# Kernel optimization log

Measured on AMD Instinct MI355X. Metric: run time of the kernel, lower is better.

Reference implementation:

```python
import jax, jax.numpy as jnp
import numpy as np


def setup_inputs() -> dict:
    key = jax.random.key(0)
    # coeffs_tensor: stacked/padded wavelet coefficients [B, F, T]
    coeffs = jax.random.normal(key, (16, 256, 8192), dtype=jnp.float32)
    return {"coeffs": coeffs}


def reference(coeffs) -> jnp.ndarray:
    B, F, T = coeffs.shape
    # torch.angle on a real tensor -> 0 for x>=0, pi for x<0; jnp.angle matches.
    phase = jnp.angle(coeffs)
    inst_freq = jnp.diff(phase, axis=-1)
    inst_freq = jnp.pad(inst_freq, ((0, 0), (0, 0), (0, 1)))  # F.pad(..., (0,1))
    freq_adjusted = jnp.clip(inst_freq, -1.0, 1.0)  # [B,F,T]
    # k = (f + freq_adjusted).long(); .long() truncates toward zero, as does astype(int32)
    f_idx = jnp.arange(F, dtype=coeffs.dtype)[None, :, None]
    k = jnp.clip((f_idx + freq_adjusted).astype(jnp.int32), 0, F - 1)  # [B,F,T]
    # Fused scatter-add over all (b, f, t): sst[b, k[b,f,t], t] += coeffs[b, f, t]
    b_idx = jnp.arange(B)[:, None, None]
    t_idx = jnp.arange(T)[None, None, :]
    sst = jnp.zeros_like(coeffs).at[b_idx, k, t_idx].add(coeffs)
    return sst
```

## Files before the change

### kernel.cpp

```cpp
#include <hip/hip_runtime.h>

typedef float f32x4 __attribute__((ext_vector_type(4)));

#define BB 16
#define FF 256
#define TT 8192
#define F_CHUNK 8
#define ROWS (F_CHUNK + 2)
#define THREADS 256
#define TBLK (THREADS * 4)
#define LROW 1024

__device__ __forceinline__ void dma16(const float* g, float* l) {
    __builtin_amdgcn_global_load_lds(
        (const __attribute__((address_space(1))) unsigned int*)g,
        (__attribute__((address_space(3))) unsigned int*)l,
        16, 0, 0);
}

__device__ __forceinline__ int sgn_bit(float x) {
    return (int)(__float_as_uint(x) >> 31);
}

__global__ __launch_bounds__(THREADS) void sst_kernel(const float* __restrict__ in,
                                                      float* __restrict__ out) {
    __shared__ float sm[ROWS][LROW];

    const int tid    = threadIdx.x;
    const int wid    = tid >> 6;
    const int blockT = blockIdx.x * TBLK;
    const int fs     = blockIdx.y * F_CHUNK;
    const int b      = blockIdx.z;

    const float* srcB = in  + (size_t)b * FF * TT + blockT;
    float*       dstB = out + (size_t)b * FF * TT + blockT;

    const bool hasNext = (blockT + TBLK) < TT;
    const bool lastThr = (tid == THREADS - 1);

    #pragma unroll
    for (int i = 0; i < ROWS; ++i) {
        int f = fs - 1 + i;
        f = f < 0 ? 0 : (f > FF - 1 ? FF - 1 : f);
        dma16(srcB + (size_t)f * TT + tid * 4, &sm[i][wid * 256]);
    }

    float eg[ROWS];
    #pragma unroll
    for (int i = 0; i < ROWS; ++i) eg[i] = 0.0f;
    if (lastThr && hasNext) {
        #pragma unroll
        for (int i = 0; i < ROWS; ++i) {
            int f = fs - 1 + i;
            f = f < 0 ? 0 : (f > FF - 1 ? FF - 1 : f);
            eg[i] = srcB[(size_t)f * TT + TBLK];
        }
    }

    asm volatile("s_waitcnt vmcnt(0)" ::: "memory");
    __syncthreads();

    const int  tid4 = tid * 4;
    const bool tail = (blockT + tid4 + 4 >= TT);
    const int  eidx = tid4 + 4 > LROW - 1 ? LROW - 1 : tid4 + 4;

    f32x4    v[ROWS];
    unsigned pk[ROWS];
    #pragma unroll
    for (int i = 0; i < ROWS; ++i) {
        const int f = fs - 1 + i;
        const bool oob = (f < 0) | (f > FF - 1);
        v[i] = *reinterpret_cast<const f32x4*>(&sm[i][tid4]);
        const float el = sm[i][eidx];
        const float e  = lastThr ? eg[i] : el;
        const int s0 = sgn_bit(v[i][0]), s1 = sgn_bit(v[i][1]),
                  s2 = sgn_bit(v[i][2]), s3 = sgn_bit(v[i][3]), s4 = sgn_bit(e);
        const int a0 = s1 - s0 + 1;
        const int a1 = s2 - s1 + 1;
        const int a2 = s3 - s2 + 1;
        const int a3 = tail ? 1 : (s4 - s3 + 1);
        pk[i] = oob ? 0x55u : (unsigned)(a0 | (a1 << 2) | (a2 << 4) | (a3 << 6));
    }

    #pragma unroll
    for (int i = 1; i <= F_CHUNK; ++i) {
        const int g = fs + (i - 1);
        const bool isFirst = (g == 0);
        const bool isLast  = (g == FF - 1);

        const unsigned pp = pk[i - 1], pc = pk[i], pn = pk[i + 1];
        const f32x4    vp = v[i - 1],  vc = v[i],  vn = v[i + 1];

        f32x4 r;
        {
            const unsigned cp = pp & 3u, cc = pc & 3u, cn = pn & 3u;
            const bool bc = (cc == 1u) || (isFirst && cc == 0u) || (isLast && cc == 2u);
            r[0] = ((cp == 2u) ? vp[0] : 0.f) + (bc ? vc[0] : 0.f) + ((cn == 0u) ? vn[0] : 0.f);
        }
        {
            const unsigned cp = (pp >> 2) & 3u, cc = (pc >> 2) & 3u, cn = (pn >> 2) & 3u;
            const bool bc = (cc == 1u) || (isFirst && cc == 0u) || (isLast && cc == 2u);
            r[1] = ((cp == 2u) ? vp[1] : 0.f) + (bc ? vc[1] : 0.f) + ((cn == 0u) ? vn[1] : 0.f);
        }
        {
            const unsigned cp = (pp >> 4) & 3u, cc = (pc >> 4) & 3u, cn = (pn >> 4) & 3u;
            const bool bc = (cc == 1u) || (isFirst && cc == 0u) || (isLast && cc == 2u);
            r[2] = ((cp == 2u) ? vp[2] : 0.f) + (bc ? vc[2] : 0.f) + ((cn == 0u) ? vn[2] : 0.f);
        }
        {
            const unsigned cp = (pp >> 6) & 3u, cc = (pc >> 6) & 3u, cn = (pn >> 6) & 3u;
            const bool bc = (cc == 1u) || (isFirst && cc == 0u) || (isLast && cc == 2u);
            r[3] = ((cp == 2u) ? vp[3] : 0.f) + (bc ? vc[3] : 0.f) + ((cn == 0u) ? vn[3] : 0.f);
        }

        __builtin_nontemporal_store(r, reinterpret_cast<f32x4*>(dstB + (size_t)g * TT + tid4));
    }
}

extern "C" void kernel_launch(void* const* d_in, const int* in_sizes, int n_in,
                              void* d_out, int out_size, void* d_ws, size_t ws_size,
                              hipStream_t stream) {
    const float* in  = (const float*)d_in[0];
    float*       out = (float*)d_out;
    dim3 grid(TT / TBLK, FF / F_CHUNK, BB);
    sst_kernel<<<grid, THREADS, 0, stream>>>(in, out);
}
```

Measured before the change: 225.5 us.

## Pipeline row loads with staged vmcnt waits and defer block-edge column fixup

The single wait for all ten row DMAs is replaced by staged waits (vmcnt 6/5/5), so early rows are processed and stored while later rows are still arriving. The last thread's extra global loads of the next column before the barrier are removed. The final column of each block is first written with a placeholder value and then recomputed by a fixup pass after all loads drain. The risk is that counting outstanding vmcnt across DMA and store operations is fragile, and the fixup adds a second store to the edge column.

```diff
diff --git a/kernel.cpp b/kernel.cpp
--- a/kernel.cpp
+++ b/kernel.cpp
@@ -9,6 +9,7 @@
 #define ROWS (F_CHUNK + 2)
 #define THREADS 256
 #define TBLK (THREADS * 4)
+#define NXBLK (TT / TBLK)
 #define LROW 1024
 
 __device__ __forceinline__ void dma16(const float* g, float* l) {
@@ -28,92 +29,99 @@
 
     const int tid    = threadIdx.x;
     const int wid    = tid >> 6;
+    const int tid4   = tid * 4;
     const int blockT = blockIdx.x * TBLK;
     const int fs     = blockIdx.y * F_CHUNK;
     const int b      = blockIdx.z;
 
-    const float* srcB = in  + (size_t)b * FF * TT + blockT;
-    float*       dstB = out + (size_t)b * FF * TT + blockT;
-
-    const bool hasNext = (blockT + TBLK) < TT;
-    const bool lastThr = (tid == THREADS - 1);
+    const float* srcRow = in  + (size_t)b * FF * TT;
+    float*       dstRow = out + (size_t)b * FF * TT;
 
     #pragma unroll
     for (int i = 0; i < ROWS; ++i) {
         int f = fs - 1 + i;
         f = f < 0 ? 0 : (f > FF - 1 ? FF - 1 : f);
-        dma16(srcB + (size_t)f * TT + tid * 4, &sm[i][wid * 256]);
+        dma16(srcRow + (size_t)f * TT + blockT + tid4, &sm[i][wid * 256]);
+        __builtin_amdgcn_sched_barrier(0);
     }
 
-    float eg[ROWS];
-    #pragma unroll
-    for (int i = 0; i < ROWS; ++i) eg[i] = 0.0f;
-    if (lastThr && hasNext) {
-        #pragma unroll
-        for (int i = 0; i < ROWS; ++i) {
-            int f = fs - 1 + i;
-            f = f < 0 ? 0 : (f > FF - 1 ? FF - 1 : f);
-            eg[i] = srcB[(size_t)f * TT + TBLK];
-        }
-    }
-
-    asm volatile("s_waitcnt vmcnt(0)" ::: "memory");
-    __syncthreads();
-
-    const int  tid4 = tid * 4;
-    const bool tail = (blockT + tid4 + 4 >= TT);
-    const int  eidx = tid4 + 4 > LROW - 1 ? LROW - 1 : tid4 + 4;
+    const int  eidx    = (tid4 + 4 > LROW - 1) ? (LROW - 1) : (tid4 + 4);
+    const bool tailThr = (blockIdx.x == NXBLK - 1) && (tid == THREADS - 1);
 
     f32x4    v[ROWS];
     unsigned pk[ROWS];
-    #pragma unroll
-    for (int i = 0; i < ROWS; ++i) {
-        const int f = fs - 1 + i;
+
+    auto finish_row = [&](int i) {
+        v[i] = *reinterpret_cast<const f32x4*>(&sm[i][tid4]);
+        const float e = sm[i][eidx];
+        const int f   = fs - 1 + i;
         const bool oob = (f < 0) | (f > FF - 1);
-        v[i] = *reinterpret_cast<const f32x4*>(&sm[i][tid4]);
-        const float el = sm[i][eidx];
-        const float e  = lastThr ? eg[i] : el;
         const int s0 = sgn_bit(v[i][0]), s1 = sgn_bit(v[i][1]),
                   s2 = sgn_bit(v[i][2]), s3 = sgn_bit(v[i][3]), s4 = sgn_bit(e);
-        const int a0 = s1 - s0 + 1;
-        const int a1 = s2 - s1 + 1;
-        const int a2 = s3 - s2 + 1;
-        const int a3 = tail ? 1 : (s4 - s3 + 1);
+        const int a0 = s1 - s0 + 1, a1 = s2 - s1 + 1, a2 = s3 - s2 + 1;
+        const int a3 = tailThr ? 1 : (s4 - s3 + 1);
         pk[i] = oob ? 0x55u : (unsigned)(a0 | (a1 << 2) | (a2 << 4) | (a3 << 6));
-    }
+    };
 
-    #pragma unroll
-    for (int i = 1; i <= F_CHUNK; ++i) {
+    auto emit_row = [&](int i) {
         const int g = fs + (i - 1);
-        const bool isFirst = (g == 0);
-        const bool isLast  = (g == FF - 1);
-
+        const bool isFirst = (g == 0), isLast = (g == FF - 1);
         const unsigned pp = pk[i - 1], pc = pk[i], pn = pk[i + 1];
         const f32x4    vp = v[i - 1],  vc = v[i],  vn = v[i + 1];
+        f32x4 r;
+        #pragma unroll
+        for (int q = 0; q < 4; ++q) {
+            const unsigned cp = (pp >> (2 * q)) & 3u;
+            const unsigned cc = (pc >> (2 * q)) & 3u;
+            const unsigned cn = (pn >> (2 * q)) & 3u;
+            const bool bc = (cc == 1u) || (isFirst && cc == 0u) || (isLast && cc == 2u);
+            r[q] = ((cp == 2u) ? vp[q] : 0.f) + (bc ? vc[q] : 0.f) + ((cn == 0u) ? vn[q] : 0.f);
+        }
+        __builtin_nontemporal_store(
+            r, reinterpret_cast<f32x4*>(dstRow + (size_t)g * TT + blockT + tid4));
+    };
 
-        f32x4 r;
-        {
-            const unsigned cp = pp & 3u, cc = pc & 3u, cn = pn & 3u;
-            const bool bc = (cc == 1u) || (isFirst && cc == 0u) || (isLast && cc == 2u);
-            r[0] = ((cp == 2u) ? vp[0] : 0.f) + (bc ? vc[0] : 0.f) + ((cn == 0u) ? vn[0] : 0.f);
+    asm volatile("s_waitcnt vmcnt(6)" ::: "memory");
+    __builtin_amdgcn_s_barrier();
+    __builtin_amdgcn_sched_barrier(0);
+    finish_row(0); finish_row(1); finish_row(2); finish_row(3);
+    emit_row(1); emit_row(2);
+
+    asm volatile("s_waitcnt vmcnt(5)" ::: "memory");
+    __builtin_amdgcn_s_barrier();
+    __builtin_amdgcn_sched_barrier(0);
+    finish_row(4); finish_row(5); finish_row(6);
+    emit_row(3); emit_row(4); emit_row(5);
+
+    asm volatile("s_waitcnt vmcnt(5)" ::: "memory");
+    __builtin_amdgcn_s_barrier();
+    __builtin_amdgcn_sched_barrier(0);
+    finish_row(7); finish_row(8); finish_row(9);
+    emit_row(6); emit_row(7); emit_row(8);
+
+    if (blockIdx.x != NXBLK - 1) {
+        asm volatile("s_waitcnt vmcnt(0)" ::: "memory");
+        __builtin_amdgcn_s_barrier();
+        __builtin_amdgcn_sched_barrier(0);
+        if (tid < F_CHUNK) {
+            const int g = fs + tid;
+            const size_t cg = (size_t)(blockT + TBLK - 1);
+            const float vpv = sm[tid][LROW - 1];
+            const float vcv = sm[tid + 1][LROW - 1];
+            const float vnv = sm[tid + 2][LROW - 1];
+            const float* nc = srcRow + cg + 1;
+            const int am = (g - 1 >= 0)
+                         ? (sgn_bit(nc[(size_t)(g - 1) * TT]) - sgn_bit(vpv)) : 9;
+            const int ac =  sgn_bit(nc[(size_t)g * TT]) - sgn_bit(vcv);
+            const int an = (g + 1 <= FF - 1)
+                         ? (sgn_bit(nc[(size_t)(g + 1) * TT]) - sgn_bit(vnv)) : 9;
+            const bool bcb = (ac == 0) || (g == 0 && ac < 0) || (g == FF - 1 && ac > 0);
+            float r = 0.f;
+            if (am == 1)  r += vpv;
+            if (bcb)      r += vcv;
+            if (an == -1) r += vnv;
+            dstRow[(size_t)g * TT + cg] = r;
         }
-        {
-            const unsigned cp = (pp >> 2) & 3u, cc = (pc >> 2) & 3u, cn = (pn >> 2) & 3u;
-            const bool bc = (cc == 1u) || (isFirst && cc == 0u) || (isLast && cc == 2u);
-            r[1] = ((cp == 2u) ? vp[1] : 0.f) + (bc ? vc[1] : 0.f) + ((cn == 0u) ? vn[1] : 0.f);
-        }
-        {
-            const unsigned cp = (pp >> 4) & 3u, cc = (pc >> 4) & 3u, cn = (pn >> 4) & 3u;
-            const bool bc = (cc == 1u) || (isFirst && cc == 0u) || (isLast && cc == 2u);
-            r[2] = ((cp == 2u) ? vp[2] : 0.f) + (bc ? vc[2] : 0.f) + ((cn == 0u) ? vn[2] : 0.f);
-        }
-        {
-            const unsigned cp = (pp >> 6) & 3u, cc = (pc >> 6) & 3u, cn = (pn >> 6) & 3u;
-            const bool bc = (cc == 1u) || (isFirst && cc == 0u) || (isLast && cc == 2u);
-            r[3] = ((cp == 2u) ? vp[3] : 0.f) + (bc ? vc[3] : 0.f) + ((cn == 0u) ? vn[3] : 0.f);
-        }
-
-        __builtin_nontemporal_store(r, reinterpret_cast<f32x4*>(dstB + (size_t)g * TT + tid4));
     }
 }
 
@@ -122,6 +130,6 @@
                               hipStream_t stream) {
     const float* in  = (const float*)d_in[0];
     float*       out = (float*)d_out;
-    dim3 grid(TT / TBLK, FF / F_CHUNK, BB);
+    dim3 grid(NXBLK, FF / F_CHUNK, BB);
     sst_kernel<<<grid, THREADS, 0, stream>>>(in, out);
 }
```

Measured after the change: 228.6 us. Within noise of the previous version (+1.4%).
